# Kernel optimization log

Measured on AMD Instinct MI355X. Metric: run time of the kernel, lower is better.

Reference implementation:

```python
import jax, jax.numpy as jnp
import numpy as np

NUM_STEPS = 5
RELAX = 1.5
EPS = 1e-5
SIZE = 128
OUT = 128
HSIZE = SIZE + OUT  # feature transformer width (256)


def bn_inf(x, g, b, m, v):
    # inference batch norm with running stats
    return g * (x - m) * jax.lax.rsqrt(v + EPS) + b


def glu(h):
    return h[:, :HSIZE] * jax.nn.sigmoid(h[:, HSIZE:])


def sparsemax(z):
    d = z.shape[-1]
    z_sorted = -jnp.sort(-z, axis=-1)  # descending
    z_cum = jnp.cumsum(z_sorted, axis=-1)
    k = jnp.arange(1, d + 1, dtype=z.dtype)
    support = 1.0 + k * z_sorted > z_cum
    k_z = jnp.sum(support, axis=-1, keepdims=True)  # int support size
    tau = (jnp.take_along_axis(z_cum, k_z - 1, axis=-1) - 1.0) / k_z.astype(z.dtype)
    return jnp.maximum(z - tau, 0.0)


def feat_transformer(x, Ws0, Ws1, Wu_t, g, b, m, v):
    # 4 GLU FeatureBlocks: blocks 0,1 use shared fc weights, 2,3 unshared
    sqrt_half = jnp.sqrt(jnp.asarray(0.5, x.dtype))
    h = glu(bn_inf(x @ Ws0, g[0], b[0], m[0], v[0]))
    h = h * sqrt_half + glu(bn_inf(h @ Ws1, g[1], b[1], m[1], v[1]))
    h = h * sqrt_half + glu(bn_inf(h @ Wu_t[0], g[2], b[2], m[2], v[2]))
    h = h * sqrt_half + glu(bn_inf(h @ Wu_t[1], g[3], b[3], m[3], v[3]))
    return h


def setup_inputs() -> dict:
    key = jax.random.key(0)
    ks = jax.random.split(key, 20)
    B, F = 32768, 512
    U = 2 * HSIZE  # GLU fc units = 512
    T = NUM_STEPS + 1
    sc = 0.05
    inp = {}
    inp['features'] = jax.random.normal(ks[0], (B, F), jnp.float32)
    inp['bn0_g'] = 1.0 + 0.1 * jax.random.normal(ks[1], (F,), jnp.float32)
    inp['bn0_b'] = 0.1 * jax.random.normal(ks[2], (F,), jnp.float32)
    inp['bn0_m'] = 0.1 * jax.random.normal(ks[3], (F,), jnp.float32)
    inp['bn0_v'] = jax.random.uniform(ks[4], (F,), jnp.float32, 0.5, 1.5)
    inp['Ws0'] = sc * jax.random.normal(ks[5], (F, U), jnp.float32)
    inp['Ws1'] = sc * jax.random.normal(ks[6], (HSIZE, U), jnp.float32)
    inp['Wu'] = sc * jax.random.normal(ks[7], (T, 2, HSIZE, U), jnp.float32)
    inp['ft_g'] = 1.0 + 0.1 * jax.random.normal(ks[8], (T, 4, U), jnp.float32)
    inp['ft_b'] = 0.1 * jax.random.normal(ks[9], (T, 4, U), jnp.float32)
    inp['ft_m'] = 0.1 * jax.random.normal(ks[10], (T, 4, U), jnp.float32)
    inp['ft_v'] = jax.random.uniform(ks[11], (T, 4, U), jnp.float32, 0.5, 1.5)
    inp['W_att'] = sc * jax.random.normal(ks[12], (NUM_STEPS, SIZE, F), jnp.float32)
    inp['att_g'] = 1.0 + 0.1 * jax.random.normal(ks[13], (NUM_STEPS, F), jnp.float32)
    inp['att_b'] = 0.1 * jax.random.normal(ks[14], (NUM_STEPS, F), jnp.float32)
    inp['att_m'] = 0.1 * jax.random.normal(ks[15], (NUM_STEPS, F), jnp.float32)
    inp['att_v'] = jax.random.uniform(ks[16], (NUM_STEPS, F), jnp.float32, 0.5, 1.5)
    inp['Wf'] = sc * jax.random.normal(ks[17], (SIZE, OUT), jnp.float32)
    inp['bf'] = jnp.zeros((OUT,), jnp.float32)
    return inp


def reference(features, bn0_g, bn0_b, bn0_m, bn0_v, Ws0, Ws1, Wu,
              ft_g, ft_b, ft_m, ft_v, W_att, att_g, att_b, att_m, att_v, Wf, bf):
    B = features.shape[0]
    feats = bn_inf(features, bn0_g, bn0_b, bn0_m, bn0_v)
    prior = jnp.ones_like(feats)
    out_acc = jnp.zeros((B, OUT), feats.dtype)
    x = feat_transformer(feats, Ws0, Ws1, Wu[0], ft_g[0], ft_b[0], ft_m[0], ft_v[0])
    masks = []
    for s in range(NUM_STEPS):
        att = bn_inf(x[:, OUT:] @ W_att[s], att_g[s], att_b[s], att_m[s], att_v[s])
        mask = sparsemax(att * prior)
        prior = prior * (RELAX - mask)
        masks.append(mask)
        x = feat_transformer(mask * feats, Ws0, Ws1, Wu[s + 1],
                             ft_g[s + 1], ft_b[s + 1], ft_m[s + 1], ft_v[s + 1])
        out_acc = out_acc + jax.nn.relu(x[:, :OUT])
    final = out_acc @ Wf + bf
    return final, jnp.stack(masks)
```

## Files before the change

kernel.cpp:

```cpp
#include <hip/hip_runtime.h>
#include <hip/hip_bf16.h>
#include <math.h>

#define B_ROWS   32768
#define NSTEPS   5
#define EPS_BN   1e-5f
#define RELAX_C  1.5f
#define SQRT_HALF 0.70710678118654752440f

typedef _Float16 f16;
typedef _Float16 f16x4 __attribute__((ext_vector_type(4)));
typedef _Float16 f16x8 __attribute__((ext_vector_type(8)));
typedef float    f32x4 __attribute__((ext_vector_type(4)));

__device__ __forceinline__ int glu_perm2(int c) {
    int g = c >> 5, o = c & 31;
    return (o < 16) ? (g * 16 + o) : (g * 16 + (o - 16) + 256);
}

__device__ __forceinline__ void gload16(const void* g, void* l) {
    __builtin_amdgcn_global_load_lds(
        (const __attribute__((address_space(1))) unsigned int*)g,
        (__attribute__((address_space(3))) unsigned int*)l, 16, 0, 0);
}

__global__ void prep_all(
    const float* __restrict__ bn0_g, const float* __restrict__ bn0_b,
    const float* __restrict__ bn0_m, const float* __restrict__ bn0_v,
    const float* __restrict__ ft_g, const float* __restrict__ ft_b,
    const float* __restrict__ ft_m, const float* __restrict__ ft_v,
    const float* __restrict__ att_g, const float* __restrict__ att_b,
    const float* __restrict__ att_m, const float* __restrict__ att_v,
    const float* __restrict__ Ws0, const float* __restrict__ Ws1,
    const float* __restrict__ Wu,  const float* __restrict__ Wat,
    const float* __restrict__ features,
    float* __restrict__ ftS, float* __restrict__ ftH,
    float* __restrict__ attS, float* __restrict__ attH,
    f16* __restrict__ ws0, f16* __restrict__ ws1,
    f16* __restrict__ wu,  f16* __restrict__ wat,
    f16* __restrict__ feats, float* __restrict__ oacc)
{
    const int blk = blockIdx.x;
    if (blk < 60) {
        int idx = blk * 256 + threadIdx.x;
        if (idx < 24 * 512) {
            int tb = idx >> 9;
            int c = idx & 511;
            int src = tb * 512 + glu_perm2(c);
            float s = ft_g[src] * rsqrtf(ft_v[src] + EPS_BN);
            ftS[idx] = s;
            ftH[idx] = ft_b[src] - ft_m[src] * s;
        } else if (idx < 24 * 512 + 5 * 512) {
            int q = idx - 24 * 512;
            float s = att_g[q] * rsqrtf(att_v[q] + EPS_BN);
            attS[q] = s;
            attH[q] = att_b[q] - att_m[q] * s;
        }
    } else if (blk < 9020) {
        int i = (blk - 60) * 256 + threadIdx.x;
        if (i < 262144) {
            int n = i >> 9, k = i & 511;
            ws0[i] = (f16)Ws0[(k << 9) + glu_perm2(n)];
        } else if (i < 393216) {
            int j = i - 262144;
            int n = j >> 8, k = j & 255;
            ws1[j] = (f16)Ws1[(k << 9) + glu_perm2(n)];
        } else if (i < 1966080) {
            int j = i - 393216;
            int mat = j >> 17;
            int r = j & 131071;
            int n = r >> 8, k = r & 255;
            wu[j] = (f16)Wu[(mat << 17) + (k << 9) + glu_perm2(n)];
        } else if (i < 2293760) {
            int j = i - 1966080;
            int mat = j >> 16;
            int r = j & 65535;
            int n = r >> 7, k = r & 127;
            wat[j] = (f16)Wat[(mat << 16) + (k << 9) + n];
        }
    } else {
        const int b = blk - 9020;
        if (b < 16384) {
            int i = b * 256 + threadIdx.x;
            int base = i * 4;
            int c = base & 511;
            float4 xv = *(const float4*)(features + base);
            f16x4 hv;
            float s0 = bn0_g[c]     * rsqrtf(bn0_v[c]     + EPS_BN);
            float s1 = bn0_g[c + 1] * rsqrtf(bn0_v[c + 1] + EPS_BN);
            float s2 = bn0_g[c + 2] * rsqrtf(bn0_v[c + 2] + EPS_BN);
            float s3 = bn0_g[c + 3] * rsqrtf(bn0_v[c + 3] + EPS_BN);
            hv.x = (f16)((xv.x - bn0_m[c])     * s0 + bn0_b[c]);
            hv.y = (f16)((xv.y - bn0_m[c + 1]) * s1 + bn0_b[c + 1]);
            hv.z = (f16)((xv.z - bn0_m[c + 2]) * s2 + bn0_b[c + 2]);
            hv.w = (f16)((xv.w - bn0_m[c + 3]) * s3 + bn0_b[c + 3]);
            *(f16x4*)(feats + base) = hv;
        } else {
            int i = (b - 16384) * 256 + threadIdx.x;
            ((float4*)oacc)[i] = make_float4(0.f, 0.f, 0.f, 0.f);
        }
    }
}

template<int MODE, int NT>
__global__ __launch_bounds__(512, 4) void gemm_conveyor(
    const f16* __restrict__ A, const int ldA,
    const f16* __restrict__ B,
    const float* __restrict__ scale, const float* __restrict__ shift,
    const f16* __restrict__ res,
    f16* __restrict__ out,
    float* __restrict__ oacc)
{
    constexpr int K = NT * 32;
    __shared__ __align__(16) char smem[3 * 24576];
    const int tid  = threadIdx.x;
    const int lane = tid & 63;
    const int w    = tid >> 6;
    const int wm   = w >> 1;
    const int wn   = w & 1;
    const int lr   = lane & 15;
    const int lh   = lane >> 4;
    const int d    = blockIdx.x;
    const int bid  = (d & 7) * 64 + (d >> 3);
    const int row0 = (bid >> 2) * 256;
    const int bcol = (bid & 3) * 128;

    const int c0 = 3 * w, c1 = 3 * w + 1, c2 = 3 * w + 2;
    const bool a0 = c0 < 16, a1 = c1 < 16, a2 = c2 < 16;
    const char* p0 = a0 ? (const char*)(A + (size_t)(row0 + c0 * 16 + lr) * ldA + lh * 8)
                        : (const char*)(B + (size_t)(bcol + (c0 - 16) * 16 + lr) * K + lh * 8);
    const char* p1 = a1 ? (const char*)(A + (size_t)(row0 + c1 * 16 + lr) * ldA + lh * 8)
                        : (const char*)(B + (size_t)(bcol + (c1 - 16) * 16 + lr) * K + lh * 8);
    const char* p2 = a2 ? (const char*)(A + (size_t)(row0 + c2 * 16 + lr) * ldA + lh * 8)
                        : (const char*)(B + (size_t)(bcol + (c2 - 16) * 16 + lr) * K + lh * 8);
    const int d0 = c0 * 1024, d1 = c1 * 1024, d2 = c2 * 1024;

    f32x4 acc[4][4];
    #pragma unroll
    for (int m = 0; m < 4; ++m)
        #pragma unroll
        for (int n = 0; n < 4; ++n)
            acc[m][n] = f32x4{0.f, 0.f, 0.f, 0.f};

    auto STAGE = [&](int s) {
        const int ko = s * 64;
        char* ring = smem + (s % 3) * 24576;
        gload16(p0 + ko, ring + d0);
        gload16(p1 + ko, ring + d1);
        gload16(p2 + ko, ring + d2);
    };

    STAGE(0); STAGE(1);

    for (int s = 0; s < NT; ++s) {
        if (s + 1 < NT) asm volatile("s_waitcnt vmcnt(3)" ::: "memory");
        else            asm volatile("s_waitcnt vmcnt(0)" ::: "memory");
        __builtin_amdgcn_s_barrier();
        asm volatile("" ::: "memory");
        if (s + 2 < NT) STAGE(s + 2);

        const char* L = smem + (s % 3) * 24576;
        f16x8 a[4], b[4];
        #pragma unroll
        for (int m = 0; m < 4; ++m)
            a[m] = *(const f16x8*)(L + (wm * 4 + m) * 1024 + lane * 16);
        #pragma unroll
        for (int n = 0; n < 4; ++n)
            b[n] = *(const f16x8*)(L + 16384 + (wn * 4 + n) * 1024 + lane * 16);
        __builtin_amdgcn_s_setprio(1);
        #pragma unroll
        for (int n = 0; n < 4; ++n)
            #pragma unroll
            for (int m = 0; m < 4; ++m)
                acc[m][n] = __builtin_amdgcn_mfma_f32_16x16x32_f16(a[m], b[n], acc[m][n], 0, 0, 0);
        __builtin_amdgcn_s_setprio(0);
    }

    const int rbase = row0 + wm * 64;
    #pragma unroll
    for (int p = 0; p < 2; ++p) {
        const int cb = bcol + wn * 64 + p * 32;
        const float sA = scale[cb + lr],      hA = shift[cb + lr];
        const float sB = scale[cb + 16 + lr], hB = shift[cb + 16 + lr];
        const int oc = (cb >> 1) + lr;
        #pragma unroll
        for (int m = 0; m < 4; ++m) {
            #pragma unroll
            for (int r = 0; r < 4; ++r) {
                const int row = rbase + m * 16 + lh * 4 + r;
                float y0 = acc[m][2 * p][r]     * sA + hA;
                float y1 = acc[m][2 * p + 1][r] * sB + hB;
                float val = y0 / (1.f + expf(-y1));
                if constexpr (MODE >= 1)
                    val += SQRT_HALF * (float)res[(size_t)row * 256 + oc];
                if constexpr (MODE <= 1) {
                    out[(size_t)row * 256 + oc] = (f16)val;
                } else {
                    if (oc < 128) {
                        if (oacc) oacc[(size_t)row * 128 + oc] += fmaxf(val, 0.f);
                    } else {
                        out[(size_t)row * 128 + (oc - 128)] = (f16)val;
                    }
                }
            }
        }
    }
}

template<int USE_PRIOR>
__global__ __launch_bounds__(512, 4) void att_sparsemax_kernel(
    const f16* __restrict__ A,
    const f16* __restrict__ Bw,
    const float* __restrict__ scale, const float* __restrict__ shift,
    const f16* __restrict__ feats,
    f16* __restrict__ prior,
    float* __restrict__ mask_out,
    f16* __restrict__ mf)
{
    __shared__ f16 attLds[64 * 512];
    const int tid  = threadIdx.x;
    const int lane = tid & 63;
    const int w    = tid >> 6;
    const int dd   = blockIdx.x;
    const int bid  = (dd & 7) * 64 + (dd >> 3);
    const int brow = bid * 64;
    const int lr   = lane & 15;
    const int lk   = (lane >> 4) * 8;

    f32x4 acc[4][4];
    #pragma unroll
    for (int m = 0; m < 4; ++m)
        #pragma unroll
        for (int n = 0; n < 4; ++n)
            acc[m][n] = f32x4{0.f, 0.f, 0.f, 0.f};

    const f16* pa = A + (size_t)(brow + lr) * 128 + lk;
    const f16* pb = Bw + (size_t)(w * 64 + lr) * 128 + lk;

    #pragma unroll
    for (int t = 0; t < 4; ++t) {
        f16x8 a[4], b[4];
        #pragma unroll
        for (int m = 0; m < 4; ++m) a[m] = *(const f16x8*)(pa + m * 16 * 128 + t * 32);
        #pragma unroll
        for (int n = 0; n < 4; ++n) b[n] = *(const f16x8*)(pb + n * 16 * 128 + t * 32);
        #pragma unroll
        for (int n = 0; n < 4; ++n)
            #pragma unroll
            for (int m = 0; m < 4; ++m)
                acc[m][n] = __builtin_amdgcn_mfma_f32_16x16x32_f16(a[m], b[n], acc[m][n], 0, 0, 0);
    }

    #pragma unroll
    for (int n = 0; n < 4; ++n) {
        const int col = w * 64 + n * 16 + lr;
        const float s = scale[col], h = shift[col];
        #pragma unroll
        for (int m = 0; m < 4; ++m) {
            const int r0 = m * 16 + (lane >> 4) * 4;
            #pragma unroll
            for (int r = 0; r < 4; ++r)
                attLds[(r0 + r) * 512 + col] = (f16)(acc[m][n][r] * s + h);
        }
    }
    __syncthreads();

    const int cb8 = lane * 8;
    for (int rr = 0; rr < 8; ++rr) {
        const int row = w * 8 + rr;
        const int grow = brow + row;
        const size_t g8 = (size_t)grow * 512 + cb8;

        float z[8], pr[8];
        f16x8 prv;
        if (USE_PRIOR) prv = *(const f16x8*)(prior + g8);
        f16x8 zv = *(const f16x8*)(&attLds[row * 512 + cb8]);
        #pragma unroll
        for (int j = 0; j < 8; ++j) {
            pr[j] = USE_PRIOR ? (float)prv[j] : 1.0f;
            z[j] = (float)zv[j] * pr[j];
        }
        float mx = z[0];
        #pragma unroll
        for (int j = 1; j < 8; ++j) mx = fmaxf(mx, z[j]);
        #pragma unroll
        for (int off = 32; off; off >>= 1) mx = fmaxf(mx, __shfl_xor(mx, off));

        float tau = mx - 1.0f;
        for (int it = 0; it < 20; ++it) {
            float s = 0.f, c = 0.f;
            #pragma unroll
            for (int j = 0; j < 8; ++j) {
                float dz = z[j] - tau;
                if (dz > 0.f) { s += dz; c += 1.f; }
            }
            #pragma unroll
            for (int off = 32; off; off >>= 1) {
                s += __shfl_xor(s, off);
                c += __shfl_xor(c, off);
            }
            float tn = tau + (s - 1.0f) / c;
            if (!(tn > tau)) break;
            tau = tn;
        }

        float mk[8];
        f16x8 pnew, mfv;
        f16x8 fv = *(const f16x8*)(feats + g8);
        #pragma unroll
        for (int j = 0; j < 8; ++j) {
            mk[j] = fmaxf(z[j] - tau, 0.f);
            pnew[j] = (f16)(pr[j] * (RELAX_C - mk[j]));
            mfv[j] = (f16)(mk[j] * (float)fv[j]);
        }
        f32x4 m0 = {mk[0], mk[1], mk[2], mk[3]};
        f32x4 m1 = {mk[4], mk[5], mk[6], mk[7]};
        __builtin_nontemporal_store(m0, (f32x4*)(mask_out + g8));
        __builtin_nontemporal_store(m1, (f32x4*)(mask_out + g8 + 4));
        *(f16x8*)(prior + g8) = pnew;
        *(f16x8*)(mf + g8) = mfv;
    }
}

__global__ __launch_bounds__(256) void gemm_f32_final(
    const float* __restrict__ A,
    const float* __restrict__ W,
    const float* __restrict__ bias,
    float* __restrict__ out)
{
    __shared__ float As[16][128];
    __shared__ float Bs[16][128];
    const int tid = threadIdx.x;
    const int tm = tid >> 4, tn = tid & 15;
    const int brow = blockIdx.x * 128;
    float acc[8][8] = {};
    for (int k0 = 0; k0 < 128; k0 += 16) {
        #pragma unroll
        for (int i = 0; i < 2; ++i) {
            int f = tid + i * 256;
            int row = f >> 2, kq = (f & 3) << 2;
            float4 av = *(const float4*)(A + (size_t)(brow + row) * 128 + k0 + kq);
            As[kq + 0][row] = av.x;
            As[kq + 1][row] = av.y;
            As[kq + 2][row] = av.z;
            As[kq + 3][row] = av.w;
            int kr = f >> 5, nq = (f & 31) << 2;
            *(float4*)(&Bs[kr][nq]) = *(const float4*)(W + (size_t)(k0 + kr) * 128 + nq);
        }
        __syncthreads();
        #pragma unroll
        for (int kk = 0; kk < 16; ++kk) {
            float a[8], b[8];
            *(float4*)(a)     = *(const float4*)(&As[kk][tm * 8]);
            *(float4*)(a + 4) = *(const float4*)(&As[kk][tm * 8 + 4]);
            *(float4*)(b)     = *(const float4*)(&Bs[kk][tn * 8]);
            *(float4*)(b + 4) = *(const float4*)(&Bs[kk][tn * 8 + 4]);
            #pragma unroll
            for (int i = 0; i < 8; ++i)
                #pragma unroll
                for (int j = 0; j < 8; ++j)
                    acc[i][j] += a[i] * b[j];
        }
        __syncthreads();
    }
    #pragma unroll
    for (int i = 0; i < 8; ++i) {
        int row = brow + tm * 8 + i;
        #pragma unroll
        for (int j = 0; j < 8; ++j)
            out[(size_t)row * 128 + tn * 8 + j] = acc[i][j] + bias[tn * 8 + j];
    }
}

extern "C" void kernel_launch(void* const* d_in, const int* in_sizes, int n_in,
                              void* d_out, int out_size, void* d_ws, size_t ws_size,
                              hipStream_t stream)
{
    const float* features = (const float*)d_in[0];
    const float* bn0_g = (const float*)d_in[1];
    const float* bn0_b = (const float*)d_in[2];
    const float* bn0_m = (const float*)d_in[3];
    const float* bn0_v = (const float*)d_in[4];
    const float* Ws0   = (const float*)d_in[5];
    const float* Ws1   = (const float*)d_in[6];
    const float* Wu    = (const float*)d_in[7];
    const float* ft_g  = (const float*)d_in[8];
    const float* ft_b  = (const float*)d_in[9];
    const float* ft_m  = (const float*)d_in[10];
    const float* ft_v  = (const float*)d_in[11];
    const float* W_att = (const float*)d_in[12];
    const float* att_g = (const float*)d_in[13];
    const float* att_b = (const float*)d_in[14];
    const float* att_m = (const float*)d_in[15];
    const float* att_v = (const float*)d_in[16];
    const float* Wf    = (const float*)d_in[17];
    const float* bf    = (const float*)d_in[18];
    float* out = (float*)d_out;

    char* wp = (char*)d_ws;
    auto alloc = [&](size_t bytes) { char* r = wp; wp += (bytes + 255) & ~(size_t)255; return r; };
    const size_t BR = B_ROWS;
    f16* feats  = (f16*)alloc(BR * 512 * 2);
    f16* mfbuf  = (f16*)alloc(BR * 512 * 2);
    f16* ubuf   = (f16*)alloc(BR * 256 * 2);
    f16* vbuf   = (f16*)alloc(BR * 256 * 2);
    f16* xhalf  = (f16*)alloc(BR * 128 * 2);
    f16* prior  = (f16*)alloc(BR * 512 * 2);
    float* oacc  = (float*)alloc(BR * 128 * 4);
    f16* ws0  = (f16*)alloc(512 * 512 * 2);
    f16* ws1  = (f16*)alloc(512 * 256 * 2);
    f16* wu   = (f16*)alloc((size_t)12 * 512 * 256 * 2);
    f16* wat  = (f16*)alloc((size_t)5 * 512 * 128 * 2);
    float* ftS  = (float*)alloc(24 * 512 * 4);
    float* ftH  = (float*)alloc(24 * 512 * 4);
    float* attS = (float*)alloc(5 * 512 * 4);
    float* attH = (float*)alloc(5 * 512 * 4);

    prep_all<<<29500, 256, 0, stream>>>(
        bn0_g, bn0_b, bn0_m, bn0_v, ft_g, ft_b, ft_m, ft_v,
        att_g, att_b, att_m, att_v, Ws0, Ws1, Wu, W_att, features,
        ftS, ftH, attS, attH, ws0, ws1, wu, wat, feats, oacc);

    auto ft = [&](const f16* in, int t, bool accum) {
        const f16* wu0 = wu + (size_t)(t * 2 + 0) * 131072;
        const f16* wu1 = wu + (size_t)(t * 2 + 1) * 131072;
        gemm_conveyor<0, 16><<<512, 512, 0, stream>>>(in, 512, ws0,
            ftS + (t * 4 + 0) * 512, ftH + (t * 4 + 0) * 512,
            nullptr, ubuf, nullptr);
        gemm_conveyor<1, 8><<<512, 512, 0, stream>>>(ubuf, 256, ws1,
            ftS + (t * 4 + 1) * 512, ftH + (t * 4 + 1) * 512,
            ubuf, vbuf, nullptr);
        gemm_conveyor<1, 8><<<512, 512, 0, stream>>>(vbuf, 256, wu0,
            ftS + (t * 4 + 2) * 512, ftH + (t * 4 + 2) * 512,
            vbuf, ubuf, nullptr);
        gemm_conveyor<2, 8><<<512, 512, 0, stream>>>(ubuf, 256, wu1,
            ftS + (t * 4 + 3) * 512, ftH + (t * 4 + 3) * 512,
            ubuf, xhalf, accum ? oacc : nullptr);
    };

    ft(feats, 0, false);

    for (int s = 0; s < NSTEPS; ++s) {
        float* mask_s = out + 4194304 + (size_t)s * 16777216;
        if (s == 0)
            att_sparsemax_kernel<0><<<512, 512, 0, stream>>>(
                xhalf, wat + (size_t)s * 65536,
                attS + s * 512, attH + s * 512,
                feats, prior, mask_s, mfbuf);
        else
            att_sparsemax_kernel<1><<<512, 512, 0, stream>>>(
                xhalf, wat + (size_t)s * 65536,
                attS + s * 512, attH + s * 512,
                feats, prior, mask_s, mfbuf);
        ft(mfbuf, s + 1, true);
    }

    gemm_f32_final<<<B_ROWS / 128, 256, 0, stream>>>(oacc, Wf, bf, out);
}
```

Measured before the change: 929.7 us.

## Switch conveyor GEMM to 32x32x16 MFMA with matching GLU column permutation

Replaces the 16x16x32 MFMA tiles in the main GEMM with 32x32x16 MFMA instructions, giving 4 accumulators of 16 floats per wave instead of 16 of 4. The weight/BN GLU permutation changes from 16-wide to 32-wide groups so the gate and value columns still land in paired accumulators, and the LDS staging and epilogue row mapping are reworked to match. It also raises wave priority around the MFMA block in the attention kernel. The larger MFMA halves instruction count and LDS fragment reuse differs, but the epilogue now does strided stores by row groups.

```diff
diff --git a/kernel.cpp b/kernel.cpp
--- a/kernel.cpp
+++ b/kernel.cpp
@@ -12,10 +12,11 @@
 typedef _Float16 f16x4 __attribute__((ext_vector_type(4)));
 typedef _Float16 f16x8 __attribute__((ext_vector_type(8)));
 typedef float    f32x4 __attribute__((ext_vector_type(4)));
-
-__device__ __forceinline__ int glu_perm2(int c) {
-    int g = c >> 5, o = c & 31;
-    return (o < 16) ? (g * 16 + o) : (g * 16 + (o - 16) + 256);
+typedef float    f32x16 __attribute__((ext_vector_type(16)));
+
+__device__ __forceinline__ int glu_perm3(int c) {
+    int g = c >> 6, o = c & 63;
+    return (o < 32) ? (g * 32 + o) : (g * 32 + (o - 32) + 256);
 }
 
 __device__ __forceinline__ void gload16(const void* g, void* l) {
@@ -46,7 +47,7 @@
         if (idx < 24 * 512) {
             int tb = idx >> 9;
             int c = idx & 511;
-            int src = tb * 512 + glu_perm2(c);
+            int src = tb * 512 + glu_perm3(c);
             float s = ft_g[src] * rsqrtf(ft_v[src] + EPS_BN);
             ftS[idx] = s;
             ftH[idx] = ft_b[src] - ft_m[src] * s;
@@ -60,17 +61,17 @@
         int i = (blk - 60) * 256 + threadIdx.x;
         if (i < 262144) {
             int n = i >> 9, k = i & 511;
-            ws0[i] = (f16)Ws0[(k << 9) + glu_perm2(n)];
+            ws0[i] = (f16)Ws0[(k << 9) + glu_perm3(n)];
         } else if (i < 393216) {
             int j = i - 262144;
             int n = j >> 8, k = j & 255;
-            ws1[j] = (f16)Ws1[(k << 9) + glu_perm2(n)];
+            ws1[j] = (f16)Ws1[(k << 9) + glu_perm3(n)];
         } else if (i < 1966080) {
             int j = i - 393216;
             int mat = j >> 17;
             int r = j & 131071;
             int n = r >> 8, k = r & 255;
-            wu[j] = (f16)Wu[(mat << 17) + (k << 9) + glu_perm2(n)];
+            wu[j] = (f16)Wu[(mat << 17) + (k << 9) + glu_perm3(n)];
         } else if (i < 2293760) {
             int j = i - 1966080;
             int mat = j >> 16;
@@ -118,29 +119,33 @@
     const int w    = tid >> 6;
     const int wm   = w >> 1;
     const int wn   = w & 1;
-    const int lr   = lane & 15;
-    const int lh   = lane >> 4;
+    const int lq   = lane & 31;
+    const int lh2  = lane >> 5;
     const int d    = blockIdx.x;
     const int bid  = (d & 7) * 64 + (d >> 3);
     const int row0 = (bid >> 2) * 256;
     const int bcol = (bid & 3) * 128;
 
     const int c0 = 3 * w, c1 = 3 * w + 1, c2 = 3 * w + 2;
-    const bool a0 = c0 < 16, a1 = c1 < 16, a2 = c2 < 16;
-    const char* p0 = a0 ? (const char*)(A + (size_t)(row0 + c0 * 16 + lr) * ldA + lh * 8)
-                        : (const char*)(B + (size_t)(bcol + (c0 - 16) * 16 + lr) * K + lh * 8);
-    const char* p1 = a1 ? (const char*)(A + (size_t)(row0 + c1 * 16 + lr) * ldA + lh * 8)
-                        : (const char*)(B + (size_t)(bcol + (c1 - 16) * 16 + lr) * K + lh * 8);
-    const char* p2 = a2 ? (const char*)(A + (size_t)(row0 + c2 * 16 + lr) * ldA + lh * 8)
-                        : (const char*)(B + (size_t)(bcol + (c2 - 16) * 16 + lr) * K + lh * 8);
+    auto gp = [&](int c) -> const char* {
+        if (c < 16)
+            return (const char*)(A + (size_t)(row0 + (c >> 1) * 32 + lq) * ldA
+                                 + (c & 1) * 16 + lh2 * 8);
+        int cc = c - 16;
+        return (const char*)(B + (size_t)(bcol + (cc >> 1) * 32 + lq) * K
+                             + (cc & 1) * 16 + lh2 * 8);
+    };
+    const char* p0 = gp(c0); const char* p1 = gp(c1); const char* p2 = gp(c2);
     const int d0 = c0 * 1024, d1 = c1 * 1024, d2 = c2 * 1024;
 
-    f32x4 acc[4][4];
-    #pragma unroll
-    for (int m = 0; m < 4; ++m)
-        #pragma unroll
-        for (int n = 0; n < 4; ++n)
-            acc[m][n] = f32x4{0.f, 0.f, 0.f, 0.f};
+    f32x16 acc[2][2];
+    #pragma unroll
+    for (int m = 0; m < 2; ++m)
+        #pragma unroll
+        for (int n = 0; n < 2; ++n)
+            #pragma unroll
+            for (int i = 0; i < 16; ++i)
+                acc[m][n][i] = 0.f;
 
     auto STAGE = [&](int s) {
         const int ko = s * 64;
@@ -160,47 +165,48 @@
         if (s + 2 < NT) STAGE(s + 2);
 
         const char* L = smem + (s % 3) * 24576;
-        f16x8 a[4], b[4];
-        #pragma unroll
-        for (int m = 0; m < 4; ++m)
-            a[m] = *(const f16x8*)(L + (wm * 4 + m) * 1024 + lane * 16);
-        #pragma unroll
-        for (int n = 0; n < 4; ++n)
-            b[n] = *(const f16x8*)(L + 16384 + (wn * 4 + n) * 1024 + lane * 16);
+        f16x8 a00 = *(const f16x8*)(L + (wm * 4 + 0) * 1024 + lane * 16);
+        f16x8 a01 = *(const f16x8*)(L + (wm * 4 + 1) * 1024 + lane * 16);
+        f16x8 a10 = *(const f16x8*)(L + (wm * 4 + 2) * 1024 + lane * 16);
+        f16x8 a11 = *(const f16x8*)(L + (wm * 4 + 3) * 1024 + lane * 16);
+        f16x8 b00 = *(const f16x8*)(L + 16384 + (wn * 4 + 0) * 1024 + lane * 16);
+        f16x8 b01 = *(const f16x8*)(L + 16384 + (wn * 4 + 1) * 1024 + lane * 16);
+        f16x8 b10 = *(const f16x8*)(L + 16384 + (wn * 4 + 2) * 1024 + lane * 16);
+        f16x8 b11 = *(const f16x8*)(L + 16384 + (wn * 4 + 3) * 1024 + lane * 16);
         __builtin_amdgcn_s_setprio(1);
-        #pragma unroll
-        for (int n = 0; n < 4; ++n)
-            #pragma unroll
-            for (int m = 0; m < 4; ++m)
-                acc[m][n] = __builtin_amdgcn_mfma_f32_16x16x32_f16(a[m], b[n], acc[m][n], 0, 0, 0);
+        acc[0][0] = __builtin_amdgcn_mfma_f32_32x32x16_f16(a00, b00, acc[0][0], 0, 0, 0);
+        acc[1][0] = __builtin_amdgcn_mfma_f32_32x32x16_f16(a10, b00, acc[1][0], 0, 0, 0);
+        acc[0][1] = __builtin_amdgcn_mfma_f32_32x32x16_f16(a00, b10, acc[0][1], 0, 0, 0);
+        acc[1][1] = __builtin_amdgcn_mfma_f32_32x32x16_f16(a10, b10, acc[1][1], 0, 0, 0);
+        acc[0][0] = __builtin_amdgcn_mfma_f32_32x32x16_f16(a01, b01, acc[0][0], 0, 0, 0);
+        acc[1][0] = __builtin_amdgcn_mfma_f32_32x32x16_f16(a11, b01, acc[1][0], 0, 0, 0);
+        acc[0][1] = __builtin_amdgcn_mfma_f32_32x32x16_f16(a01, b11, acc[0][1], 0, 0, 0);
+        acc[1][1] = __builtin_amdgcn_mfma_f32_32x32x16_f16(a11, b11, acc[1][1], 0, 0, 0);
         __builtin_amdgcn_s_setprio(0);
     }
 
-    const int rbase = row0 + wm * 64;
-    #pragma unroll
-    for (int p = 0; p < 2; ++p) {
-        const int cb = bcol + wn * 64 + p * 32;
-        const float sA = scale[cb + lr],      hA = shift[cb + lr];
-        const float sB = scale[cb + 16 + lr], hB = shift[cb + 16 + lr];
-        const int oc = (cb >> 1) + lr;
-        #pragma unroll
-        for (int m = 0; m < 4; ++m) {
-            #pragma unroll
-            for (int r = 0; r < 4; ++r) {
-                const int row = rbase + m * 16 + lh * 4 + r;
-                float y0 = acc[m][2 * p][r]     * sA + hA;
-                float y1 = acc[m][2 * p + 1][r] * sB + hB;
-                float val = y0 / (1.f + expf(-y1));
-                if constexpr (MODE >= 1)
-                    val += SQRT_HALF * (float)res[(size_t)row * 256 + oc];
-                if constexpr (MODE <= 1) {
-                    out[(size_t)row * 256 + oc] = (f16)val;
+    const int cb = bcol + wn * 64;
+    const float sA = scale[cb + lq],      hA = shift[cb + lq];
+    const float sB = scale[cb + 32 + lq], hB = shift[cb + 32 + lq];
+    const int oc = (cb >> 1) + lq;
+    #pragma unroll
+    for (int m = 0; m < 2; ++m) {
+        const int rbase = row0 + wm * 64 + m * 32 + 4 * lh2;
+        #pragma unroll
+        for (int reg = 0; reg < 16; ++reg) {
+            const int row = rbase + (reg & 3) + 8 * (reg >> 2);
+            float y0 = acc[m][0][reg] * sA + hA;
+            float y1 = acc[m][1][reg] * sB + hB;
+            float val = y0 / (1.f + expf(-y1));
+            if constexpr (MODE >= 1)
+                val += SQRT_HALF * (float)res[(size_t)row * 256 + oc];
+            if constexpr (MODE <= 1) {
+                out[(size_t)row * 256 + oc] = (f16)val;
+            } else {
+                if (oc < 128) {
+                    if (oacc) oacc[(size_t)row * 128 + oc] += fmaxf(val, 0.f);
                 } else {
-                    if (oc < 128) {
-                        if (oacc) oacc[(size_t)row * 128 + oc] += fmaxf(val, 0.f);
-                    } else {
-                        out[(size_t)row * 128 + (oc - 128)] = (f16)val;
-                    }
+                    out[(size_t)row * 128 + (oc - 128)] = (f16)val;
                 }
             }
         }
@@ -244,11 +250,13 @@
         for (int m = 0; m < 4; ++m) a[m] = *(const f16x8*)(pa + m * 16 * 128 + t * 32);
         #pragma unroll
         for (int n = 0; n < 4; ++n) b[n] = *(const f16x8*)(pb + n * 16 * 128 + t * 32);
+        __builtin_amdgcn_s_setprio(1);
         #pragma unroll
         for (int n = 0; n < 4; ++n)
             #pragma unroll
             for (int m = 0; m < 4; ++m)
                 acc[m][n] = __builtin_amdgcn_mfma_f32_16x16x32_f16(a[m], b[n], acc[m][n], 0, 0, 0);
+        __builtin_amdgcn_s_setprio(0);
     }
 
     #pragma unroll
```

After: 963.1 us. +3.6%, slower.
